# Kernel tuning notes

Measured on AMD Instinct MI355X. Metric: run time of the kernel, lower is better.

Reference implementation:

```python
import jax, jax.numpy as jnp
import numpy as np

jax.config.update("jax_enable_x64", True)

NUM_OF_LSB_TO_IGNORE = 5
COMPARISON_NUM_BITS_IGNORED = 5
SCALE = 65536.0  # activations live on an integer-share-like scale so bit shifts matter

BLOCK_SIZES = np.array([[0, 1]] * 32 + [[2, 2]] * 48 + [[4, 4]] * 48)
# active (non-identity) block sizes and the channel indices they own
ACTIVE = [(tuple(int(v) for v in bs), np.where(np.all(BLOCK_SIZES == bs, axis=1))[0])
          for bs in np.unique(BLOCK_SIZES, axis=0) if 0 not in bs]


def setup_inputs() -> dict:
    key = jax.random.key(0)
    activation = jax.random.normal(key, (16, 128, 114, 114), dtype=jnp.float32) * SCALE
    return {"activation": activation}


def _block_sign(x, bh, bw):
    # x: [N, c, H, W]. Pad bottom/right to block multiples, space-to-depth,
    # integer floor-mean per block, LSB truncation via int16 wrap, sign >= 0.
    N, c, H, W = x.shape
    ph, pw = (-H) % bh, (-W) % bw
    xp = jnp.pad(x, ((0, 0), (0, 0), (0, ph), (0, pw)))
    xr = xp.reshape(N, c, (H + ph) // bh, bh, (W + pw) // bw, bw)
    s = xr.sum(axis=(3, 5)).astype(jnp.int64)          # block sums
    mean = s // (bh * bw)                               # integer floor mean
    q = ((mean >> NUM_OF_LSB_TO_IGNORE).astype(jnp.int16)
         .astype(jnp.int64)) << COMPARISON_NUM_BITS_IGNORED
    sign = q >= 0                                       # DReLU
    # broadcast block sign back to pixels, then unpad
    sign = jnp.repeat(jnp.repeat(sign, bh, axis=2), bw, axis=3)
    return sign[:, :, :H, :W]


def reference(activation):
    out = activation
    for (bh, bw), ch in ACTIVE:  # small fixed set of block-size groups
        cur = activation[:, ch]
        sign = _block_sign(cur, bh, bw)
        out = out.at[:, ch].set(cur * sign.astype(activation.dtype))
    return out
```

## Files before the change

kernel.cpp:

```cpp
#include <hip/hip_runtime.h>


typedef float v4 __attribute__((ext_vector_type(4)));

#define PLANE 12996
#define P4 3249
#define WS4_BASE 2495232

__global__ __launch_bounds__(256) void mask_kernel(const float* __restrict__ in,
                                                   unsigned char* __restrict__ ws) {
    __shared__ float Lp[PLANE];
    const int wg  = blockIdx.x;
    const int n   = wg / 96;
    const int cr  = wg - n * 96;
    const int tid = threadIdx.x;
    const v4* __restrict__ ip = (const v4*)(in + (size_t)(n * 128 + 32 + cr) * PLANE);

    v4 r[12];
#pragma unroll
    for (int i = 0; i < 12; ++i) r[i] = ip[tid + 256 * i];
    v4 rt;
    if (tid < 177) rt = ip[tid + 3072];
#pragma unroll
    for (int i = 0; i < 12; ++i) *(v4*)&Lp[4 * (tid + 256 * i)] = r[i];
    if (tid < 177) *(v4*)&Lp[4 * (tid + 3072)] = rt;
    __syncthreads();

    if (cr < 48) {
        unsigned char* mp = ws + (size_t)(n * 48 + cr) * 3249;
        for (int b = tid; b < 3249; b += 256) {
            int bh = b / 57, bw = b - bh * 57;
            const float* p = &Lp[228 * bh + 2 * bw];
            float s = ((p[0] + p[1]) + p[114]) + p[115];
            mp[b] = (s > -1.0f) ? 1 : 0;
        }
    } else {
        unsigned char* mp = ws + WS4_BASE + (size_t)(n * 48 + (cr - 48)) * 841;
        for (int b = tid; b < 841; b += 256) {
            int bh = b / 29, bw = b - bh * 29;
            int h0 = 4 * bh, w0 = 4 * bw;
            int nh = (bh == 28) ? 2 : 4;
            int nw = (bw == 28) ? 2 : 4;
            float s = 0.0f;
            for (int r2 = 0; r2 < nh; ++r2) {
                const float* p = &Lp[(h0 + r2) * 114 + w0];
                for (int j = 0; j < nw; ++j) s += p[j];
            }
            mp[b] = (s > -1.0f) ? 1 : 0;
        }
    }
}

__global__ __launch_bounds__(256) void apply_kernel(const float* __restrict__ in,
                                                    const unsigned char* __restrict__ ws,
                                                    float* __restrict__ out) {
    const int i = blockIdx.x * 256 + threadIdx.x;
    v4 v = ((const v4*)in)[i];
    int plane = i / P4;
    int rr    = i - plane * P4;
    int c     = plane & 127;
    v4 o;
    if (c < 32) {
        o = v;
    } else {
        int q = 4 * rr;
        int h = q / 114;
        int w = q - h * 114;
        if (c < 80) {
            const unsigned char* mp = ws + (size_t)((plane >> 7) * 48 + (c - 32)) * 3249;
#pragma unroll
            for (int e = 0; e < 4; ++e) {
                o[e] = v[e] * (float)mp[(h >> 1) * 57 + (w >> 1)];
                if (++w == 114) { w = 0; ++h; }
            }
        } else {
            const unsigned char* mp = ws + WS4_BASE + (size_t)((plane >> 7) * 48 + (c - 80)) * 841;
#pragma unroll
            for (int e = 0; e < 4; ++e) {
                o[e] = v[e] * (float)mp[(h >> 2) * 29 + (w >> 2)];
                if (++w == 114) { w = 0; ++h; }
            }
        }
    }
    __builtin_nontemporal_store(o, &((v4*)out)[i]);
}

extern "C" void kernel_launch(void* const* d_in, const int* in_sizes, int n_in,
                              void* d_out, int out_size, void* d_ws, size_t ws_size,
                              hipStream_t stream) {
    const float* in = (const float*)d_in[0];
    float* out = (float*)d_out;
    unsigned char* ws = (unsigned char*)d_ws;
    mask_kernel<<<1536, 256, 0, stream>>>(in, ws);
    apply_kernel<<<25992, 256, 0, stream>>>(in, ws, out);
}
```

Baseline: 195.3 us.

## Rewrite mask kernel as direct-global grid-stride loop and batch apply loads

The mask kernel no longer stages whole channel planes through LDS. Each thread now reads its block rows straight from global memory with vector loads and writes two mask bytes at a time into padded, row-strided mask buffers. The apply kernel becomes a persistent-style kernel that issues four independent float4 loads per iteration across a fixed grid, and each float4 now needs only two mask lookups instead of four. It also drops the nontemporal store hint. The aim is to cut LDS traffic and launch and tail overhead and to raise memory-level parallelism, at the risk of less coalesced mask-kernel reads and of output stores now polluting the cache.

```diff
diff --git a/kernel.cpp b/kernel.cpp
--- a/kernel.cpp
+++ b/kernel.cpp
@@ -2,87 +2,146 @@
 
 
 typedef float v4 __attribute__((ext_vector_type(4)));
+typedef float v2 __attribute__((ext_vector_type(2)));
 
 #define PLANE 12996
 #define P4 3249
-#define WS4_BASE 2495232
+#define M2STRIDE 64
+#define M2PLANE 3648
+#define M4STRIDE 32
+#define M4PLANE 928
+#define M4OFF 2801664
+#define T2 1269504
+#define T4 334080
+#define TT (T2 + T4)
 
 __global__ __launch_bounds__(256) void mask_kernel(const float* __restrict__ in,
                                                    unsigned char* __restrict__ ws) {
-    __shared__ float Lp[PLANE];
-    const int wg  = blockIdx.x;
-    const int n   = wg / 96;
-    const int cr  = wg - n * 96;
-    const int tid = threadIdx.x;
-    const v4* __restrict__ ip = (const v4*)(in + (size_t)(n * 128 + 32 + cr) * PLANE);
-
-    v4 r[12];
-#pragma unroll
-    for (int i = 0; i < 12; ++i) r[i] = ip[tid + 256 * i];
-    v4 rt;
-    if (tid < 177) rt = ip[tid + 3072];
-#pragma unroll
-    for (int i = 0; i < 12; ++i) *(v4*)&Lp[4 * (tid + 256 * i)] = r[i];
-    if (tid < 177) *(v4*)&Lp[4 * (tid + 3072)] = rt;
-    __syncthreads();
-
-    if (cr < 48) {
-        unsigned char* mp = ws + (size_t)(n * 48 + cr) * 3249;
-        for (int b = tid; b < 3249; b += 256) {
-            int bh = b / 57, bw = b - bh * 57;
-            const float* p = &Lp[228 * bh + 2 * bw];
-            float s = ((p[0] + p[1]) + p[114]) + p[115];
-            mp[b] = (s > -1.0f) ? 1 : 0;
-        }
-    } else {
-        unsigned char* mp = ws + WS4_BASE + (size_t)(n * 48 + (cr - 48)) * 841;
-        for (int b = tid; b < 841; b += 256) {
-            int bh = b / 29, bw = b - bh * 29;
-            int h0 = 4 * bh, w0 = 4 * bw;
-            int nh = (bh == 28) ? 2 : 4;
-            int nw = (bw == 28) ? 2 : 4;
-            float s = 0.0f;
-            for (int r2 = 0; r2 < nh; ++r2) {
-                const float* p = &Lp[(h0 + r2) * 114 + w0];
-                for (int j = 0; j < nw; ++j) s += p[j];
+    const int G = 1024 * 256;
+    for (int u = blockIdx.x * 256 + threadIdx.x; u < TT; u += G) {
+        if (u < T2) {
+            int p = u / 1653;
+            int rest = u - p * 1653;
+            int r = rest / 29;
+            int j = rest - r * 29;
+            int n = p / 48, cr = p - n * 48;
+            const float* bp = in + (size_t)(n * 128 + 32 + cr) * PLANE + 228 * r;
+            unsigned char* mp = ws + (size_t)p * M2PLANE + M2STRIDE * r;
+            if (j < 28) {
+                int w0 = 4 * j;
+                v4 a  = *(const v4*)(bp + w0);
+                v2 b0 = *(const v2*)(bp + w0 + 114);
+                v2 b1 = *(const v2*)(bp + w0 + 116);
+                float s0 = ((a.x + a.y) + b0.x) + b0.y;
+                float s1 = ((a.z + a.w) + b1.x) + b1.y;
+                unsigned short m = (unsigned short)((s0 > -1.0f) ? 1 : 0)
+                                 | (unsigned short)(((s1 > -1.0f) ? 1 : 0) << 8);
+                *(unsigned short*)(mp + 2 * j) = m;
+            } else {
+                v2 a = *(const v2*)(bp + 112);
+                v2 b = *(const v2*)(bp + 226);
+                float s = ((a.x + a.y) + b.x) + b.y;
+                mp[56] = (s > -1.0f) ? 1 : 0;
             }
-            mp[b] = (s > -1.0f) ? 1 : 0;
+        } else {
+            int v = u - T2;
+            int p = v / 435;
+            int rest = v - p * 435;
+            int r = rest / 15;
+            int jp = rest - r * 15;
+            int n = p / 48, cr = p - n * 48;
+            const float* bp = in + (size_t)(n * 128 + 80 + cr) * PLANE;
+            unsigned char* mp = ws + M4OFF + (size_t)p * M4PLANE + M4STRIDE * r;
+            int h0 = 4 * r;
+            int nh = (r == 28) ? 2 : 4;
+            if (jp < 14) {
+                int w0 = 8 * jp;
+                float s0 = 0.0f, s1 = 0.0f;
+                for (int k = 0; k < nh; ++k) {
+                    const float* rp = bp + (h0 + k) * 114 + w0;
+                    if ((k & 1) == 0) {
+                        v4 x = *(const v4*)rp;
+                        v4 y = *(const v4*)(rp + 4);
+                        s0 = (((s0 + x.x) + x.y) + x.z) + x.w;
+                        s1 = (((s1 + y.x) + y.y) + y.z) + y.w;
+                    } else {
+                        v2 x0 = *(const v2*)rp;
+                        v2 x1 = *(const v2*)(rp + 2);
+                        v2 y0 = *(const v2*)(rp + 4);
+                        v2 y1 = *(const v2*)(rp + 6);
+                        s0 = (((s0 + x0.x) + x0.y) + x1.x) + x1.y;
+                        s1 = (((s1 + y0.x) + y0.y) + y1.x) + y1.y;
+                    }
+                }
+                unsigned short m = (unsigned short)((s0 > -1.0f) ? 1 : 0)
+                                 | (unsigned short)(((s1 > -1.0f) ? 1 : 0) << 8);
+                *(unsigned short*)(mp + 2 * jp) = m;
+            } else {
+                float s = 0.0f;
+                for (int k = 0; k < nh; ++k) {
+                    v2 x = *(const v2*)(bp + (h0 + k) * 114 + 112);
+                    s = (s + x.x) + x.y;
+                }
+                mp[28] = (s > -1.0f) ? 1 : 0;
+            }
         }
     }
+}
+
+#define G2 524288
+#define N4 6653952
+
+__device__ __forceinline__ v4 apply_one(int i, v4 v, const unsigned char* __restrict__ ws) {
+    int plane = i / P4;
+    int rr = i - plane * P4;
+    int c = plane & 127;
+    if (c < 32) return v;
+    int q = 4 * rr;
+    int h = q / 114;
+    int w0 = q - h * 114;
+    int i0, i1;
+    const unsigned char* mb;
+    if (c < 80) {
+        mb = ws + (size_t)((plane >> 7) * 48 + (c - 32)) * M2PLANE;
+        i0 = M2STRIDE * (h >> 1) + (w0 >> 1);
+        i1 = (w0 <= 110) ? (M2STRIDE * (h >> 1) + ((w0 + 2) >> 1))
+                         : (M2STRIDE * ((h + 1) >> 1));
+    } else {
+        mb = ws + M4OFF + (size_t)((plane >> 7) * 48 + (c - 80)) * M4PLANE;
+        i0 = M4STRIDE * (h >> 2) + (w0 >> 2);
+        i1 = (w0 <= 110) ? (M4STRIDE * (h >> 2) + ((w0 + 2) >> 2))
+                         : (M4STRIDE * ((h + 1) >> 2));
+    }
+    float m0 = (float)mb[i0];
+    float m1 = (float)mb[i1];
+    v4 o;
+    o.x = v.x * m0; o.y = v.y * m0; o.z = v.z * m1; o.w = v.w * m1;
+    return o;
 }
 
 __global__ __launch_bounds__(256) void apply_kernel(const float* __restrict__ in,
                                                     const unsigned char* __restrict__ ws,
                                                     float* __restrict__ out) {
-    const int i = blockIdx.x * 256 + threadIdx.x;
-    v4 v = ((const v4*)in)[i];
-    int plane = i / P4;
-    int rr    = i - plane * P4;
-    int c     = plane & 127;
-    v4 o;
-    if (c < 32) {
-        o = v;
-    } else {
-        int q = 4 * rr;
-        int h = q / 114;
-        int w = q - h * 114;
-        if (c < 80) {
-            const unsigned char* mp = ws + (size_t)((plane >> 7) * 48 + (c - 32)) * 3249;
+    const v4* __restrict__ ip = (const v4*)in;
+    v4* __restrict__ op = (v4*)out;
+    const int base = blockIdx.x * 256 + threadIdx.x;
 #pragma unroll
-            for (int e = 0; e < 4; ++e) {
-                o[e] = v[e] * (float)mp[(h >> 1) * 57 + (w >> 1)];
-                if (++w == 114) { w = 0; ++h; }
-            }
-        } else {
-            const unsigned char* mp = ws + WS4_BASE + (size_t)((plane >> 7) * 48 + (c - 80)) * 841;
-#pragma unroll
-            for (int e = 0; e < 4; ++e) {
-                o[e] = v[e] * (float)mp[(h >> 2) * 29 + (w >> 2)];
-                if (++w == 114) { w = 0; ++h; }
-            }
-        }
+    for (int g = 0; g < 3; ++g) {
+        int i0 = base + (4 * g) * G2;
+        v4 a = ip[i0];
+        v4 b = ip[i0 + G2];
+        v4 cc = ip[i0 + 2 * G2];
+        v4 d = ip[i0 + 3 * G2];
+        op[i0]          = apply_one(i0,          a,  ws);
+        op[i0 + G2]     = apply_one(i0 + G2,     b,  ws);
+        op[i0 + 2 * G2] = apply_one(i0 + 2 * G2, cc, ws);
+        op[i0 + 3 * G2] = apply_one(i0 + 3 * G2, d,  ws);
     }
-    __builtin_nontemporal_store(o, &((v4*)out)[i]);
+    int it = base + 12 * G2;
+    if (it < N4) {
+        v4 v = ip[it];
+        op[it] = apply_one(it, v, ws);
+    }
 }
 
 extern "C" void kernel_launch(void* const* d_in, const int* in_sizes, int n_in,
@@ -91,6 +150,6 @@
     const float* in = (const float*)d_in[0];
     float* out = (float*)d_out;
     unsigned char* ws = (unsigned char*)d_ws;
-    mask_kernel<<<1536, 256, 0, stream>>>(in, ws);
-    apply_kernel<<<25992, 256, 0, stream>>>(in, ws, out);
+    mask_kernel<<<1024, 256, 0, stream>>>(in, ws);
+    apply_kernel<<<2048, 256, 0, stream>>>(in, ws, out);
 }
```

New measurement: 203.1 us. 4.0% more time.
